# Performance work log

Hardware: AMD Instinct MI355X
Metric: run time of the kernel (lower is better)

Reference implementation:

```python
import jax, jax.numpy as jnp
import numpy as np

B, S, H, NH, HD = 4, 2048, 1024, 16, 64
ROPE_BASE = 10000.0


def _rope_cos_sin(seq_len, head_dim, dtype):
    inv_freq = 1.0 / (ROPE_BASE ** (jnp.arange(0, head_dim, 2, dtype=jnp.float32) / head_dim))
    t = jnp.arange(seq_len, dtype=jnp.float32)
    freqs = jnp.einsum('i,j->ij', t, inv_freq)          # [S, HD/2]
    emb = jnp.concatenate([freqs, freqs], axis=-1)      # [S, HD]
    return emb.astype(dtype), None  # placeholder (cos/sin computed by caller)


def _rotate_half(x):
    x1, x2 = jnp.split(x, 2, axis=-1)
    return jnp.concatenate([-x2, x1], axis=-1)


def setup_inputs() -> dict:
    key = jax.random.key(0)
    k0, k1, k2, k3, k4 = jax.random.split(key, 5)
    std = 0.02
    return {
        'hidden_states': jax.random.normal(k0, (B, S, H), dtype=jnp.float32),
        'Wq': jax.random.normal(k1, (H, H), dtype=jnp.float32) * std,
        'Wk': jax.random.normal(k2, (H, H), dtype=jnp.float32) * std,
        'Wv': jax.random.normal(k3, (H, H), dtype=jnp.float32) * std,
        'Wo': jax.random.normal(k4, (H, H), dtype=jnp.float32) * std,
    }


def reference(hidden_states, Wq, Wk, Wv, Wo):
    b, s, h = hidden_states.shape
    nh, hd = NH, HD
    # QKV projections (nn.Linear: x @ W.T), reshape to [B, NH, S, HD]
    def proj(W):
        y = jnp.einsum('bsh,oh->bso', hidden_states, W)
        return y.reshape(b, s, nh, hd).transpose(0, 2, 1, 3)
    q, k, v = proj(Wq), proj(Wk), proj(Wv)

    # RoPE
    emb, _ = _rope_cos_sin(s, hd, hidden_states.dtype)  # [S, HD] angles
    cos = jnp.cos(emb)[None, None, :, :]
    sin = jnp.sin(emb)[None, None, :, :]
    q = q * cos + _rotate_half(q) * sin
    k = k * cos + _rotate_half(k) * sin

    # Manual attention path: full (unmasked) softmax attention
    scale = 1.0 / np.sqrt(hd)
    attn_weights = jnp.einsum('bhqd,bhkd->bhqk', q, k) * scale
    attn_weights = jax.nn.softmax(attn_weights, axis=-1)
    attn_output = jnp.einsum('bhqk,bhkd->bhqd', attn_weights, v)

    # Merge heads and output projection
    attn_output = attn_output.transpose(0, 2, 1, 3).reshape(b, s, h)
    return jnp.einsum('bsh,oh->bso', attn_output, Wo)
```

## Files before the change

### kernel.cpp

```cpp
#include <hip/hip_runtime.h>
#include <hip/hip_bf16.h>
#include <stdint.h>
#include <cmath>

typedef unsigned short u16;
typedef __attribute__((ext_vector_type(8))) short bf16x8;
typedef __attribute__((ext_vector_type(4))) float f32x4;
typedef __attribute__((ext_vector_type(16))) float f32x16;

#define DEVI static __device__ __forceinline__

constexpr int S_LEN = 2048;
constexpr int NHEAD = 16;
constexpr int HDIM  = 64;
constexpr int HID   = 1024;
constexpr int MROWS = 4 * 2048;

DEVI u16 f2bf(float x) {
  union { float f; uint32_t u; } a; a.f = x;
  uint32_t r = a.u + 0x7fffu + ((a.u >> 16) & 1u);
  return (u16)(r >> 16);
}

DEVI void gload16(const void* g, void* l) {
  __builtin_amdgcn_global_load_lds((const __attribute__((address_space(1))) void*)g,
                                   (__attribute__((address_space(3))) void*)l, 16, 0, 0);
}

DEVI void waitvm0_barrier() {
  asm volatile("s_waitcnt vmcnt(0)" ::: "memory");
  __builtin_amdgcn_s_barrier();
}

DEVI float xchg_max(float x) { return fmaxf(x, __shfl_xor(x, 32)); }
DEVI float xchg_add(float x) { return x + __shfl_xor(x, 32); }

DEVI uint32_t cvtpk(float lo, float hi) {
  uint32_t r;
  asm("v_cvt_pk_bf16_f32 %0, %1, %2" : "=v"(r) : "v"(lo), "v"(hi));
  return r;
}

DEVI float tmax2(const f32x16& x, const f32x16& y) {
  float m[16];
#pragma unroll
  for (int i = 0; i < 16; ++i) m[i] = fmaxf(x[i], y[i]);
#pragma unroll
  for (int s = 8; s > 0; s >>= 1)
#pragma unroll
    for (int i = 0; i < s; ++i) m[i] = fmaxf(m[i], m[i + s]);
  return m[0];
}
DEVI float tsum2(const f32x16& x, const f32x16& y) {
  float m[16];
#pragma unroll
  for (int i = 0; i < 16; ++i) m[i] = x[i] + y[i];
#pragma unroll
  for (int s = 8; s > 0; s >>= 1)
#pragma unroll
    for (int i = 0; i < s; ++i) m[i] = m[i] + m[i + s];
  return m[0];
}

__global__ void k_cvt(const float* __restrict__ src, u16* __restrict__ dst, int n4) {
  int stride = gridDim.x * blockDim.x;
  for (int i = blockIdx.x * blockDim.x + threadIdx.x; i < n4; i += stride) {
    float4 v = reinterpret_cast<const float4*>(src)[i];
    ushort4 o;
    o.x = f2bf(v.x); o.y = f2bf(v.y); o.z = f2bf(v.z); o.w = f2bf(v.w);
    reinterpret_cast<ushort4*>(dst)[i] = o;
  }
}

__global__ void k_cvtw(const float* __restrict__ Wq, const float* __restrict__ Wk,
                       const float* __restrict__ Wv, const float* __restrict__ Wo,
                       u16* __restrict__ Wqkv, u16* __restrict__ Wobf) {
  constexpr int Q4 = (HID * HID) / 4;
  int i = blockIdx.x * blockDim.x + threadIdx.x;
  int mat = i >> 18, loc = i & (Q4 - 1);
  const float* src = (mat == 0) ? Wq : (mat == 1) ? Wk : (mat == 2) ? Wv : Wo;
  u16* dst = (mat < 3) ? (Wqkv + mat * HID * HID) : Wobf;
  float4 v = reinterpret_cast<const float4*>(src)[loc];
  ushort4 o;
  o.x = f2bf(v.x); o.y = f2bf(v.y); o.z = f2bf(v.z); o.w = f2bf(v.w);
  reinterpret_cast<ushort4*>(dst)[loc] = o;
}

DEVI void gemm_ml(const u16* __restrict__ A, const u16* __restrict__ Bm,
                  int brow, int bcol, u16* As, u16* Bs, f32x4 acc[4][4]) {
  const int tid = threadIdx.x;
  const int wid = tid >> 6, lane = tid & 63;
  const int lr = lane & 15, lg = lane >> 4;
  const int wr = wid >> 1, wc = wid & 1;

#define GEMM_STAGE(KT, BUF)                                                              \
  _Pragma("unroll")                                                                      \
  for (int c = 0; c < 2; ++c) {                                                          \
    int e = c * 2048 + tid * 8;                                                          \
    int row = e >> 5, kk = e & 31;                                                       \
    gload16(A  + (size_t)(brow + row) * HID + (KT) * 32 + kk,                            \
            As + (BUF) * 4096 + c * 2048 + wid * 512);                                   \
    gload16(Bm + (size_t)(bcol + row) * HID + (KT) * 32 + kk,                            \
            Bs + (BUF) * 4096 + c * 2048 + wid * 512);                                   \
  }

  GEMM_STAGE(0, 0);
  waitvm0_barrier();
  int cur = 0;
  for (int kt = 0; kt < HID / 32; ++kt) {
    if (kt + 1 < HID / 32) { GEMM_STAGE(kt + 1, cur ^ 1); }
    const u16* Ac = As + cur * 4096;
    const u16* Bc = Bs + cur * 4096;
    bf16x8 af[4], bv[4];
#pragma unroll
    for (int m = 0; m < 4; ++m)
      af[m] = *reinterpret_cast<const bf16x8*>(Ac + (wr * 64 + m * 16 + lr) * 32 + lg * 8);
#pragma unroll
    for (int n = 0; n < 4; ++n)
      bv[n] = *reinterpret_cast<const bf16x8*>(Bc + (wc * 64 + n * 16 + lr) * 32 + lg * 8);
#pragma unroll
    for (int m = 0; m < 4; ++m)
#pragma unroll
      for (int n = 0; n < 4; ++n)
        acc[m][n] = __builtin_amdgcn_mfma_f32_16x16x32_bf16(af[m], bv[n], acc[m][n], 0, 0, 0);
    waitvm0_barrier();
    cur ^= 1;
  }
#undef GEMM_STAGE
}

DEVI void xcd_remap(int& bx, int& by) {
  int nx = gridDim.x, ny = gridDim.y;
  int nwg = nx * ny;
  int flat = blockIdx.y * nx + blockIdx.x;
  int w = (flat & 7) * (nwg >> 3) + (flat >> 3);
  bx = w / ny;
  by = w % ny;
}

__global__ __launch_bounds__(256) void k_gemm_qkv(const u16* __restrict__ X, const u16* __restrict__ W,
                                                  u16* __restrict__ Qb, u16* __restrict__ Kb,
                                                  u16* __restrict__ Vt) {
  __shared__ __align__(16) u16 As[2 * 128 * 32];
  __shared__ __align__(16) u16 Bs[2 * 128 * 32];
  f32x4 acc[4][4] = {};
  int bx, by;
  xcd_remap(bx, by);
  const int brow = bx * 128, bcol = by * 128;
  gemm_ml(X, W, brow, bcol, As, Bs, acc);

  const int tid = threadIdx.x, wid = tid >> 6, lane = tid & 63;
  const int lr = lane & 15, lg = lane >> 4;
  const int wr = wid >> 1, wc = wid & 1;
  const int colbase = bcol + wc * 64;
  const int mat = colbase >> 10;
  const int h = (colbase & 1023) >> 6;
  const float qsc = (mat == 0) ? 0.125f * 1.4426950408889634f : 1.0f;

  if (mat < 2) {
    u16* dst = (mat == 0) ? Qb : Kb;
    const float L2B = 13.287712379549449f / 32.0f;
    const float inv0 = exp2f(-(float)lr * L2B);
    const float inv1 = exp2f(-(float)(16 + lr) * L2B);
#pragma unroll
    for (int m = 0; m < 4; ++m) {
#pragma unroll
      for (int r = 0; r < 4; ++r) {
        int grow = brow + wr * 64 + m * 16 + lg * 4 + r;
        int b = grow >> 11, s = grow & 2047;
        float s0, c0, s1, c1;
        __sincosf((float)s * inv0, &s0, &c0);
        __sincosf((float)s * inv1, &s1, &c1);
        float v0 = acc[m][0][r], v1 = acc[m][1][r], v2 = acc[m][2][r], v3 = acc[m][3][r];
        float r0 = (v0 * c0 - v2 * s0) * qsc;
        float r1 = (v1 * c1 - v3 * s1) * qsc;
        float r2 = (v2 * c0 + v0 * s0) * qsc;
        float r3 = (v3 * c1 + v1 * s1) * qsc;
        size_t base = (((size_t)(b * NHEAD + h)) * S_LEN + s) * HDIM;
        dst[base + 0 * 16 + lr] = f2bf(r0);
        dst[base + 1 * 16 + lr] = f2bf(r1);
        dst[base + 2 * 16 + lr] = f2bf(r2);
        dst[base + 3 * 16 + lr] = f2bf(r3);
      }
    }
  } else {
#pragma unroll
    for (int m = 0; m < 4; ++m) {
      int g0 = brow + wr * 64 + m * 16 + lg * 4;
      int b = g0 >> 11, s0 = g0 & 2047;
#pragma unroll
      for (int n = 0; n < 4; ++n) {
        int d = n * 16 + lr;
        ushort4 o;
        o.x = f2bf(acc[m][n][0]); o.y = f2bf(acc[m][n][1]);
        o.z = f2bf(acc[m][n][2]); o.w = f2bf(acc[m][n][3]);
        *reinterpret_cast<ushort4*>(
            Vt + (((size_t)(b * NHEAD + h)) * HDIM + d) * S_LEN + s0) = o;
      }
    }
  }
}

__global__ __launch_bounds__(128, 2) void k_attn(const u16* __restrict__ Qb, const u16* __restrict__ Kb,
                                                 const u16* __restrict__ Vt, u16* __restrict__ Ob) {
  __shared__ __align__(16) u16 Klds[2 * 64 * 64];
  __shared__ __align__(16) u16 Vlds[2 * 64 * 64];
  const int flat = blockIdx.y * 16 + blockIdx.x;
  const int xcd = flat & 7, idx = flat >> 3;
  const int bh = (xcd << 3) | (idx >> 4);
  const int qt = idx & 15;
  const int tid = threadIdx.x, wid = tid >> 6, lane = tid & 63;
  const int l31 = lane & 31, lhi = lane >> 5;
  const u16* Qp = Qb + (size_t)bh * S_LEN * HDIM;
  const u16* Kp = Kb + (size_t)bh * S_LEN * HDIM;
  const u16* Vp = Vt + (size_t)bh * HDIM * S_LEN;

  bf16x8 qf[2][4];
#pragma unroll
  for (int u = 0; u < 2; ++u) {
    const int qrow = qt * 128 + wid * 64 + u * 32 + l31;
#pragma unroll
    for (int dc = 0; dc < 4; ++dc)
      qf[u][dc] = *reinterpret_cast<const bf16x8*>(Qp + (size_t)qrow * HDIM + dc * 16 + lhi * 8);
  }

  f32x16 o[2][2] = {};
  float mrun[2] = { -INFINITY, -INFINITY };
  float lrun[2] = { 0.f, 0.f };

#define ATTN_STAGE(KV0, BUF)                                                             \
  _Pragma("unroll")                                                                      \
  for (int c = 0; c < 4; ++c) {                                                          \
    int ob = c * 2048 + tid * 16;                                                        \
    int row = ob >> 7;                                                                   \
    int srcb = ob ^ ((row & 7) << 4);                                                    \
    int colel = (srcb & 127) >> 1;                                                       \
    gload16(Kp + (size_t)((KV0) + row) * HDIM + colel,                                   \
            (u16*)((char*)Klds + (BUF) * 8192 + c * 2048 + wid * 1024));                 \
    gload16(Vp + (size_t)row * S_LEN + (KV0) + colel,                                    \
            (u16*)((char*)Vlds + (BUF) * 8192 + c * 2048 + wid * 1024));                 \
  }

  ATTN_STAGE(0, 0);
  waitvm0_barrier();
  int cur = 0;

  for (int kv0 = 0; kv0 < S_LEN; kv0 += 64) {
    if (kv0 + 64 < S_LEN) { ATTN_STAGE(kv0 + 64, cur ^ 1); }
    const char* Kc = (char*)Klds + cur * 8192;
    const char* Vc = (char*)Vlds + cur * 8192;

    f32x16 st[2][2] = {};
    __builtin_amdgcn_s_setprio(1);
#pragma unroll
    for (int dc = 0; dc < 4; ++dc) {
#pragma unroll
      for (int t = 0; t < 2; ++t) {
        int row = t * 32 + l31;
        int byteoff = (row * 128 + dc * 32 + lhi * 16) ^ ((row & 7) << 4);
        bf16x8 bk = *reinterpret_cast<const bf16x8*>(Kc + byteoff);
        st[0][t] = __builtin_amdgcn_mfma_f32_32x32x16_bf16(bk, qf[0][dc], st[0][t], 0, 0, 0);
        st[1][t] = __builtin_amdgcn_mfma_f32_32x32x16_bf16(bk, qf[1][dc], st[1][t], 0, 0, 0);
      }
    }
    __builtin_amdgcn_s_setprio(0);

    float tm[2];
#pragma unroll
    for (int u = 0; u < 2; ++u) tm[u] = xchg_max(tmax2(st[u][0], st[u][1]));

    if (__any((tm[0] > mrun[0] + 8.f) || (tm[1] > mrun[1] + 8.f))) {
#pragma unroll
      for (int u = 0; u < 2; ++u) {
        float mn = fmaxf(mrun[u], tm[u]);
        float al = __builtin_amdgcn_exp2f(mrun[u] - mn);
        mrun[u] = mn;
        lrun[u] *= al;
#pragma unroll
        for (int r = 0; r < 16; ++r) {
          float alv = __shfl(al, (r & 3) + 8 * (r >> 2) + 4 * lhi);
          o[u][0][r] *= alv;
          o[u][1][r] *= alv;
        }
      }
    }

#pragma unroll
    for (int u = 0; u < 2; ++u) {
#pragma unroll
      for (int t = 0; t < 2; ++t)
#pragma unroll
        for (int r = 0; r < 16; ++r)
          st[u][t][r] = __builtin_amdgcn_exp2f(st[u][t][r] - mrun[u]);
      lrun[u] += xchg_add(tsum2(st[u][0], st[u][1]));
    }

    __builtin_amdgcn_s_setprio(1);
#pragma unroll
    for (int t = 0; t < 2; ++t)
#pragma unroll
      for (int h2 = 0; h2 < 2; ++h2) {
        union { uint32_t w[4]; bf16x8 v; } pu[2];
#pragma unroll
        for (int u = 0; u < 2; ++u)
#pragma unroll
          for (int w = 0; w < 4; ++w)
            pu[u].w[w] = cvtpk(st[u][t][h2 * 8 + 2 * w], st[u][t][h2 * 8 + 2 * w + 1]);
#pragma unroll
        for (int n = 0; n < 2; ++n) {
          int d = n * 32 + l31;
          int X = d * 128 + t * 64 + h2 * 32 + lhi * 8;
          int sw = (d & 7) << 4;
          union { uint64_t q[2]; bf16x8 v; } bu;
          bu.q[0] = *reinterpret_cast<const uint64_t*>(Vc + (X ^ sw));
          bu.q[1] = *reinterpret_cast<const uint64_t*>(Vc + ((X | 16) ^ sw));
          o[0][n] = __builtin_amdgcn_mfma_f32_32x32x16_bf16(pu[0].v, bu.v, o[0][n], 0, 0, 0);
          o[1][n] = __builtin_amdgcn_mfma_f32_32x32x16_bf16(pu[1].v, bu.v, o[1][n], 0, 0, 0);
        }
      }
    __builtin_amdgcn_s_setprio(0);

    waitvm0_barrier();
    cur ^= 1;
  }
#undef ATTN_STAGE

  const int b = bh >> 4, h = bh & 15;
#pragma unroll
  for (int u = 0; u < 2; ++u) {
    const float linv = 1.0f / lrun[u];
#pragma unroll
    for (int r = 0; r < 16; ++r) {
      int qr = (r & 3) + 8 * (r >> 2) + 4 * lhi;
      float lv = __shfl(linv, qr);
      int s = qt * 128 + wid * 64 + u * 32 + qr;
#pragma unroll
      for (int n = 0; n < 2; ++n) {
        int d = n * 32 + l31;
        Ob[(((size_t)b * S_LEN + s) * NHEAD + h) * HDIM + d] = f2bf(o[u][n][r] * lv);
      }
    }
  }
}

__global__ __launch_bounds__(256) void k_gemm_out(const u16* __restrict__ Aa, const u16* __restrict__ Wo,
                                                  float* __restrict__ out) {
  __shared__ __align__(16) u16 As[2 * 128 * 32];
  __shared__ __align__(16) u16 Bs[2 * 128 * 32];
  f32x4 acc[4][4] = {};
  int bx, by;
  xcd_remap(bx, by);
  const int brow = bx * 128, bcol = by * 128;
  gemm_ml(Aa, Wo, brow, bcol, As, Bs, acc);

  const int tid = threadIdx.x, wid = tid >> 6, lane = tid & 63;
  const int lr = lane & 15, lg = lane >> 4;
  const int wr = wid >> 1, wc = wid & 1;
#pragma unroll
  for (int m = 0; m < 4; ++m)
#pragma unroll
    for (int n = 0; n < 4; ++n)
#pragma unroll
      for (int r = 0; r < 4; ++r) {
        int grow = brow + wr * 64 + m * 16 + lg * 4 + r;
        int gcol = bcol + wc * 64 + n * 16 + lr;
        out[(size_t)grow * HID + gcol] = acc[m][n][r];
      }
}

extern "C" void kernel_launch(void* const* d_in, const int* in_sizes, int n_in,
                              void* d_out, int out_size, void* d_ws, size_t ws_size,
                              hipStream_t stream) {
  const float* hs = (const float*)d_in[0];
  const float* Wq = (const float*)d_in[1];
  const float* Wk = (const float*)d_in[2];
  const float* Wv = (const float*)d_in[3];
  const float* Wo = (const float*)d_in[4];

  char* ws = (char*)d_ws;
  u16* Xbf  = (u16*)(ws);
  u16* Wqkv = (u16*)(ws + 16777216);
  u16* Wobf = (u16*)(ws + 23068672);
  u16* Qb   = (u16*)(ws + 25165824);
  u16* Kb   = (u16*)(ws + 41943040);
  u16* Vt   = (u16*)(ws + 58720256);
  u16* AO   = (u16*)(ws + 75497472);

  k_cvt<<<2048, 256, 0, stream>>>(hs, Xbf, (MROWS * HID) / 4);
  k_cvtw<<<4096, 256, 0, stream>>>(Wq, Wk, Wv, Wo, Wqkv, Wobf);

  k_gemm_qkv<<<dim3(MROWS / 128, 3072 / 128), 256, 0, stream>>>(Xbf, Wqkv, Qb, Kb, Vt);
  k_attn<<<dim3(S_LEN / 128, 4 * NHEAD), 128, 0, stream>>>(Qb, Kb, Vt, AO);
  k_gemm_out<<<dim3(MROWS / 128, HID / 128), 256, 0, stream>>>(AO, Wobf, (float*)d_out);
}
```

Baseline: 218.1 us.

## Triple-buffer GEMM LDS pipeline, merge conversion kernels, drop attention setprio

Switches the shared GEMM mainloop from double to triple buffering, keeping two K-tiles of global loads in flight and waiting with a partial vmcnt so load latency overlaps the MFMA work. It also merges the activation and weight fp32-to-bf16 conversion kernels into one launch, and removes the s_setprio hints around the MFMA sections in attention. The cost is more LDS per GEMM block (48KB instead of 32KB), which may lower occupancy. The vmcnt(4) value assumes exactly four outstanding loads per stage.

```diff
diff --git a/kernel.cpp b/kernel.cpp
--- a/kernel.cpp
+++ b/kernel.cpp
@@ -62,24 +62,22 @@
   return m[0];
 }
 
-__global__ void k_cvt(const float* __restrict__ src, u16* __restrict__ dst, int n4) {
-  int stride = gridDim.x * blockDim.x;
-  for (int i = blockIdx.x * blockDim.x + threadIdx.x; i < n4; i += stride) {
-    float4 v = reinterpret_cast<const float4*>(src)[i];
-    ushort4 o;
-    o.x = f2bf(v.x); o.y = f2bf(v.y); o.z = f2bf(v.z); o.w = f2bf(v.w);
-    reinterpret_cast<ushort4*>(dst)[i] = o;
-  }
-}
-
-__global__ void k_cvtw(const float* __restrict__ Wq, const float* __restrict__ Wk,
-                       const float* __restrict__ Wv, const float* __restrict__ Wo,
-                       u16* __restrict__ Wqkv, u16* __restrict__ Wobf) {
+__global__ void k_cvtall(const float* __restrict__ hs,
+                         const float* __restrict__ Wq, const float* __restrict__ Wk,
+                         const float* __restrict__ Wv, const float* __restrict__ Wo,
+                         u16* __restrict__ Xbf, u16* __restrict__ Wqkv, u16* __restrict__ Wobf) {
+  constexpr int NX = (MROWS * HID) / 4;
   constexpr int Q4 = (HID * HID) / 4;
   int i = blockIdx.x * blockDim.x + threadIdx.x;
-  int mat = i >> 18, loc = i & (Q4 - 1);
-  const float* src = (mat == 0) ? Wq : (mat == 1) ? Wk : (mat == 2) ? Wv : Wo;
-  u16* dst = (mat < 3) ? (Wqkv + mat * HID * HID) : Wobf;
+  const float* src; u16* dst; int loc;
+  if (i < NX) {
+    src = hs; dst = Xbf; loc = i;
+  } else {
+    int j = i - NX;
+    int mat = j >> 18; loc = j & (Q4 - 1);
+    src = (mat == 0) ? Wq : (mat == 1) ? Wk : (mat == 2) ? Wv : Wo;
+    dst = (mat < 3) ? (Wqkv + mat * HID * HID) : Wobf;
+  }
   float4 v = reinterpret_cast<const float4*>(src)[loc];
   ushort4 o;
   o.x = f2bf(v.x); o.y = f2bf(v.y); o.z = f2bf(v.z); o.w = f2bf(v.w);
@@ -92,6 +90,7 @@
   const int wid = tid >> 6, lane = tid & 63;
   const int lr = lane & 15, lg = lane >> 4;
   const int wr = wid >> 1, wc = wid & 1;
+  constexpr int NT = HID / 32;
 
 #define GEMM_STAGE(KT, BUF)                                                              \
   _Pragma("unroll")                                                                      \
@@ -105,10 +104,13 @@
   }
 
   GEMM_STAGE(0, 0);
-  waitvm0_barrier();
+  GEMM_STAGE(1, 1);
+  asm volatile("s_waitcnt vmcnt(4)" ::: "memory");
+  __builtin_amdgcn_s_barrier();
   int cur = 0;
-  for (int kt = 0; kt < HID / 32; ++kt) {
-    if (kt + 1 < HID / 32) { GEMM_STAGE(kt + 1, cur ^ 1); }
+  for (int kt = 0; kt < NT; ++kt) {
+    int b2 = (cur == 0) ? 2 : cur - 1;
+    if (kt + 2 < NT) { GEMM_STAGE(kt + 2, b2); }
     const u16* Ac = As + cur * 4096;
     const u16* Bc = Bs + cur * 4096;
     bf16x8 af[4], bv[4];
@@ -123,8 +125,12 @@
 #pragma unroll
       for (int n = 0; n < 4; ++n)
         acc[m][n] = __builtin_amdgcn_mfma_f32_16x16x32_bf16(af[m], bv[n], acc[m][n], 0, 0, 0);
-    waitvm0_barrier();
-    cur ^= 1;
+    if (kt + 1 < NT) {
+      if (kt + 2 < NT) asm volatile("s_waitcnt vmcnt(4)" ::: "memory");
+      else             asm volatile("s_waitcnt vmcnt(0)" ::: "memory");
+      __builtin_amdgcn_s_barrier();
+    }
+    cur = (cur == 2) ? 0 : cur + 1;
   }
 #undef GEMM_STAGE
 }
@@ -141,8 +147,8 @@
 __global__ __launch_bounds__(256) void k_gemm_qkv(const u16* __restrict__ X, const u16* __restrict__ W,
                                                   u16* __restrict__ Qb, u16* __restrict__ Kb,
                                                   u16* __restrict__ Vt) {
-  __shared__ __align__(16) u16 As[2 * 128 * 32];
-  __shared__ __align__(16) u16 Bs[2 * 128 * 32];
+  __shared__ __align__(16) u16 As[3 * 128 * 32];
+  __shared__ __align__(16) u16 Bs[3 * 128 * 32];
   f32x4 acc[4][4] = {};
   int bx, by;
   xcd_remap(bx, by);
@@ -251,7 +257,6 @@
     const char* Vc = (char*)Vlds + cur * 8192;
 
     f32x16 st[2][2] = {};
-    __builtin_amdgcn_s_setprio(1);
 #pragma unroll
     for (int dc = 0; dc < 4; ++dc) {
 #pragma unroll
@@ -263,7 +268,6 @@
         st[1][t] = __builtin_amdgcn_mfma_f32_32x32x16_bf16(bk, qf[1][dc], st[1][t], 0, 0, 0);
       }
     }
-    __builtin_amdgcn_s_setprio(0);
 
     float tm[2];
 #pragma unroll
@@ -295,7 +299,6 @@
       lrun[u] += xchg_add(tsum2(st[u][0], st[u][1]));
     }
 
-    __builtin_amdgcn_s_setprio(1);
 #pragma unroll
     for (int t = 0; t < 2; ++t)
 #pragma unroll
@@ -318,7 +321,6 @@
           o[1][n] = __builtin_amdgcn_mfma_f32_32x32x16_bf16(pu[1].v, bu.v, o[1][n], 0, 0, 0);
         }
       }
-    __builtin_amdgcn_s_setprio(0);
 
     waitvm0_barrier();
     cur ^= 1;
@@ -345,8 +347,8 @@
 
 __global__ __launch_bounds__(256) void k_gemm_out(const u16* __restrict__ Aa, const u16* __restrict__ Wo,
                                                   float* __restrict__ out) {
-  __shared__ __align__(16) u16 As[2 * 128 * 32];
-  __shared__ __align__(16) u16 Bs[2 * 128 * 32];
+  __shared__ __align__(16) u16 As[3 * 128 * 32];
+  __shared__ __align__(16) u16 Bs[3 * 128 * 32];
   f32x4 acc[4][4] = {};
   int bx, by;
   xcd_remap(bx, by);
@@ -386,8 +388,8 @@
   u16* Vt   = (u16*)(ws + 58720256);
   u16* AO   = (u16*)(ws + 75497472);
 
-  k_cvt<<<2048, 256, 0, stream>>>(hs, Xbf, (MROWS * HID) / 4);
-  k_cvtw<<<4096, 256, 0, stream>>>(Wq, Wk, Wv, Wo, Wqkv, Wobf);
+  constexpr int CVT_N = (MROWS * HID) / 4 + HID * HID;
+  k_cvtall<<<CVT_N / 256, 256, 0, stream>>>(hs, Wq, Wk, Wv, Wo, Xbf, Wqkv, Wobf);
 
   k_gemm_qkv<<<dim3(MROWS / 128, 3072 / 128), 256, 0, stream>>>(Xbf, Wqkv, Qb, Kb, Vt);
   k_attn<<<dim3(S_LEN / 128, 4 * NHEAD), 128, 0, stream>>>(Qb, Kb, Vt, AO);
```

After: 223.0 us. +2.3%, slower.
